# Performance work log

Hardware: AMD Instinct MI355X
Metric: run time of the kernel (lower is better)

The kernel has to match this reference:

```python
import jax, jax.numpy as jnp
import numpy as np

T, N = 256, 4096
H = 32
Z_SIZE, Z_CLS = 8, 8
A_SIZE, A_CLS = 4, 4
X_SIZE, X_CLS = 5, 2
E = X_SIZE * X_CLS  # embedder output = flatten(x[t]) -> 10, matches e_size
ZA = Z_SIZE * Z_CLS + A_SIZE * A_CLS  # GRUCell input size = 80


def setup_inputs() -> dict:
    key = jax.random.key(0)
    ks = jax.random.split(key, 10)
    s = 0.1
    u = jax.random.uniform(ks[3], (T, N, Z_SIZE, Z_CLS), jnp.float32, 1e-6, 1.0 - 1e-6)
    return {
        "x": jax.random.normal(ks[0], (T, N, X_SIZE, X_CLS), jnp.float32),
        "a": jax.random.normal(ks[1], (T, N, A_SIZE, A_CLS), jnp.float32),
        "h0": jax.random.normal(ks[2], (N, H), jnp.float32),
        "gumbel": -jnp.log(-jnp.log(u)),  # gumbel-max noise for OneHotCategorical sampling
        "W_ih": jax.random.normal(ks[4], (3 * H, ZA), jnp.float32) * s,
        "b_ih": jnp.zeros((3 * H,), jnp.float32),
        "W_hh": jax.random.normal(ks[5], (3 * H, H), jnp.float32) * s,
        "b_hh": jnp.zeros((3 * H,), jnp.float32),
        "W_enc": jax.random.normal(ks[6], (Z_SIZE * Z_CLS, H + E), jnp.float32) * s,
        "b_enc": jnp.zeros((Z_SIZE * Z_CLS,), jnp.float32),
        "W_dec": jax.random.normal(ks[7], (X_SIZE * X_CLS, H + Z_SIZE * Z_CLS), jnp.float32) * s,
        "b_dec": jnp.zeros((X_SIZE * X_CLS,), jnp.float32),
    }


def _gru(xin, h, W_ih, b_ih, W_hh, b_hh):
    # torch.nn.GRUCell semantics
    gi = xin @ W_ih.T + b_ih
    gh = h @ W_hh.T + b_hh
    i_r, i_z, i_n = jnp.split(gi, 3, axis=-1)
    h_r, h_z, h_n = jnp.split(gh, 3, axis=-1)
    r = jax.nn.sigmoid(i_r + h_r)
    z = jax.nn.sigmoid(i_z + h_z)
    n = jnp.tanh(i_n + r * h_n)
    return (1.0 - z) * n + z * h


def _encode(h, e, g, W_enc, b_enc):
    # encoder linear -> [N, z_size, z_cls] logits -> straight-through one-hot sample
    logits = (jnp.concatenate([h, e], axis=-1) @ W_enc.T + b_enc)
    logits = logits.reshape(h.shape[0], Z_SIZE, Z_CLS)
    idx = jnp.argmax(logits + g, axis=-1)  # gumbel-max categorical sample
    one_hot = jax.nn.one_hot(idx, Z_CLS, dtype=logits.dtype)
    probs = jax.nn.softmax(logits, axis=-1)
    return one_hot + probs - jax.lax.stop_gradient(probs)


def reference(x, a, h0, gumbel, W_ih, b_ih, W_hh, b_hh, W_enc, b_enc, W_dec, b_dec):
    z0 = _encode(h0, x[0].reshape(N, -1), gumbel[0], W_enc, b_enc)

    def step(carry, inp):
        h, z = carry
        x_t, a_prev, g_t = inp
        za = jnp.concatenate([z.reshape(N, -1), a_prev.reshape(N, -1)], axis=-1)
        h_new = _gru(za, h, W_ih, b_ih, W_hh, b_hh)
        z_new = _encode(h_new, x_t.reshape(N, -1), g_t, W_enc, b_enc)
        return (h_new, z_new), (h_new, z_new)

    _, (hs, zs) = jax.lax.scan(step, (h0, z0), (x[1:], a[:-1], gumbel[1:]))
    h_all = jnp.concatenate([h0[None], hs], axis=0)          # [T, N, H]
    z_all = jnp.concatenate([z0[None], zs], axis=0)          # [T, N, z_size, z_cls]
    hz = jnp.concatenate([h_all, z_all.reshape(T, N, -1)], axis=-1)
    x_logits = (hz @ W_dec.T + b_dec).reshape(T, N, X_SIZE, X_CLS)
    return x_logits, h_all, z_all
```

## Files before the change

kernel.cpp:

```cpp
#include <hip/hip_runtime.h>
#include <math.h>

#define T_STEPS 256
#define NB 4096

__global__ __launch_bounds__(256, 2)
void rssm_kernel(const float* __restrict__ X, const float* __restrict__ A,
                 const float* __restrict__ H0, const float* __restrict__ G,
                 const float* __restrict__ Wih, const float* __restrict__ bih,
                 const float* __restrict__ Whh, const float* __restrict__ bhh,
                 const float* __restrict__ Wenc, const float* __restrict__ benc,
                 const float* __restrict__ Wdec, const float* __restrict__ bdec,
                 float* __restrict__ out)
{
    __shared__ float  sWihz[96][65];
    __shared__ float  sWiha[96][17];
    __shared__ float  sWhh [96][33];
    __shared__ float  sWenchT[32][64];
    __shared__ float  sWenceT[10][64];
    __shared__ float  sWdech[10][37];
    __shared__ float  sWdecz[10][65];
    __shared__ double sHd[8][33];

    const int tid = threadIdx.x;
    const int i   = tid & 31;
    const int e   = tid >> 5;
    const int n   = blockIdx.x * 8 + e;

    for (int idx = tid; idx < 96*64; idx += 256){ int r = idx >> 6, c = idx & 63; sWihz[r][c] = Wih[r*80 + c]; }
    for (int idx = tid; idx < 96*16; idx += 256){ int r = idx >> 4, k = idx & 15; sWiha[r][k] = Wih[r*80 + 64 + k]; }
    for (int idx = tid; idx < 96*32; idx += 256){ int r = idx >> 5, k = idx & 31; sWhh[r][k] = Whh[r*32 + k]; }
    for (int idx = tid; idx < 32*64; idx += 256){ int k = idx >> 6, j = idx & 63; sWenchT[k][j] = Wenc[j*42 + k]; }
    for (int idx = tid; idx < 10*64; idx += 256){ int k = idx >> 6, j = idx & 63; sWenceT[k][j] = Wenc[j*42 + 32 + k]; }
    for (int idx = tid; idx < 10*32; idx += 256){ int o = idx >> 5, k = idx & 31; sWdech[o][k] = Wdec[o*96 + k]; }
    for (int idx = tid; idx < 10*64; idx += 256){ int o = idx >> 6, c = idx & 63; sWdecz[o][c] = Wdec[o*96 + 32 + c]; }
    __syncthreads();

    const double br  = (double)bih[i]      + (double)bhh[i];
    const double bz  = (double)bih[32+i]   + (double)bhh[32+i];
    const double bni = (double)bih[64+i];
    const double bnh = (double)bhh[64+i];
    const double be0 = (double)benc[2*i], be1 = (double)benc[2*i+1];
    const float  bd  = (i < 10) ? bdec[i] : 0.0f;
    const int    drow = (i < 10) ? i : 9;

    double hown = (double)H0[(size_t)n * 32 + i];
    sHd[e][i] = hown;

    int zsel[8];

    const size_t HOFF = (size_t)T_STEPS * NB * 10;
    const size_t ZOFF = HOFF + (size_t)T_STEPS * NB * 32;
    const int base = tid & 32;

    float2 g2;  float ex[10];  float ar[16] = {};
    g2 = *reinterpret_cast<const float2*>(G + (size_t)n*64 + 2*i);
    {
        const float* xr = X + (size_t)n*10;
        #pragma unroll
        for (int c = 0; c < 5; ++c){
            float2 v = *reinterpret_cast<const float2*>(xr + 2*c);
            ex[2*c] = v.x; ex[2*c+1] = v.y;
        }
    }

    #pragma unroll 1
    for (int t = 0; t < T_STEPS; ++t){
        const size_t tn = (size_t)t * NB + n;

        const int tp = (t + 1 < T_STEPS) ? t + 1 : t;
        const size_t tpn = (size_t)tp * NB + n;
        float2 g2n = *reinterpret_cast<const float2*>(G + tpn*64 + 2*i);
        float exn[10];
        {
            const float* xr = X + tpn*10;
            #pragma unroll
            for (int c = 0; c < 5; ++c){
                float2 v = *reinterpret_cast<const float2*>(xr + 2*c);
                exn[2*c] = v.x; exn[2*c+1] = v.y;
            }
        }
        float arn[16];
        {
            const float4* arow = reinterpret_cast<const float4*>(A + tn*16);
            #pragma unroll
            for (int c = 0; c < 4; ++c){
                float4 v = arow[c];
                arn[4*c+0]=v.x; arn[4*c+1]=v.y; arn[4*c+2]=v.z; arn[4*c+3]=v.w;
            }
        }

        if (t > 0){
            double gr = br, gz = bz, gn = bni, hn = bnh;
            #pragma unroll
            for (int g = 0; g < 8; ++g){
                int col = zsel[g];
                gr += (double)sWihz[i][col];
                gz += (double)sWihz[32+i][col];
                gn += (double)sWihz[64+i][col];
            }
            #pragma unroll
            for (int k = 0; k < 16; ++k){
                double ak = (double)ar[k];
                gr = fma((double)sWiha[i][k],    ak, gr);
                gz = fma((double)sWiha[32+i][k], ak, gz);
                gn = fma((double)sWiha[64+i][k], ak, gn);
            }
            #pragma unroll
            for (int k = 0; k < 32; ++k){
                double hk = sHd[e][k];
                gr = fma((double)sWhh[i][k],    hk, gr);
                gz = fma((double)sWhh[32+i][k], hk, gz);
                hn = fma((double)sWhh[64+i][k], hk, hn);
            }
            double r   = 1.0 / (1.0 + exp(-gr));
            double zg  = 1.0 / (1.0 + exp(-gz));
            double arg = gn + r * hn;
            double e2  = exp(2.0 * arg);
            double nn  = 1.0 - 2.0 / (e2 + 1.0);
            hown = (1.0 - zg) * nn + zg * hown;

            sHd[e][i] = hown;
        }

        out[HOFF + tn*32 + i] = (float)hown;

        double l0 = be0, l1 = be1;
        double dacc = (double)bd;
        #pragma unroll
        for (int k = 0; k < 32; ++k){
            double hk = sHd[e][k];
            float2 w = *reinterpret_cast<const float2*>(&sWenchT[k][2*i]);
            l0 = fma((double)w.x, hk, l0);
            l1 = fma((double)w.y, hk, l1);
            dacc = fma((double)sWdech[drow][k], hk, dacc);
        }
        #pragma unroll
        for (int k = 0; k < 10; ++k){
            float2 w = *reinterpret_cast<const float2*>(&sWenceT[k][2*i]);
            double ek = (double)ex[k];
            l0 = fma((double)w.x, ek, l0);
            l1 = fma((double)w.y, ek, l1);
        }
        double y0 = l0 + (double)g2.x, y1 = l1 + (double)g2.y;
        double m; int idxv;
        if (y1 > y0){ m = y1; idxv = 2*i + 1; } else { m = y0; idxv = 2*i; }
        #pragma unroll
        for (int d = 1; d <= 2; d <<= 1){
            double mo = __shfl_xor(m, d, 64);
            int    io = __shfl_xor(idxv, d, 64);
            if (mo > m || (mo == m && io < idxv)){ m = mo; idxv = io; }
        }

        {
            float2 zv;
            zv.x = (idxv == 2*i    ) ? 1.0f : 0.0f;
            zv.y = (idxv == 2*i + 1) ? 1.0f : 0.0f;
            *reinterpret_cast<float2*>(out + ZOFF + tn*64 + 2*i) = zv;
        }

        #pragma unroll
        for (int g = 0; g < 8; ++g){
            zsel[g] = __shfl(idxv, base + 4*g, 64);
        }

        if (i < 10){
            double acc = dacc;
            #pragma unroll
            for (int g = 0; g < 8; ++g) acc += (double)sWdecz[i][zsel[g]];
            out[tn*10 + i] = (float)acc;
        }

        g2 = g2n;
        #pragma unroll
        for (int k = 0; k < 10; ++k) ex[k] = exn[k];
        #pragma unroll
        for (int k = 0; k < 16; ++k) ar[k] = arn[k];
    }
}

extern "C" void kernel_launch(void* const* d_in, const int* in_sizes, int n_in,
                              void* d_out, int out_size, void* d_ws, size_t ws_size,
                              hipStream_t stream)
{
    const float *x   = (const float*)d_in[0];
    const float *a   = (const float*)d_in[1];
    const float *h0  = (const float*)d_in[2];
    const float *g   = (const float*)d_in[3];
    const float *wih = (const float*)d_in[4];
    const float *bih = (const float*)d_in[5];
    const float *whh = (const float*)d_in[6];
    const float *bhh = (const float*)d_in[7];
    const float *wenc= (const float*)d_in[8];
    const float *benc= (const float*)d_in[9];
    const float *wdec= (const float*)d_in[10];
    const float *bdec= (const float*)d_in[11];

    if (n_in == 12) {
        const float *b96a = nullptr, *b96b = nullptr;
        const float *tx=nullptr,*ta=nullptr,*th0=nullptr,*tg=nullptr,*twih=nullptr,
                    *twhh=nullptr,*twenc=nullptr,*tbenc=nullptr,*twdec=nullptr,*tbdec=nullptr;
        for (int k = 0; k < 12; ++k) {
            const float* p = (const float*)d_in[k];
            switch (in_sizes[k]) {
                case 10485760: tx = p;    break;
                case 16777216: ta = p;    break;
                case 131072:   th0 = p;   break;
                case 67108864: tg = p;    break;
                case 7680:     twih = p;  break;
                case 3072:     twhh = p;  break;
                case 2688:     twenc = p; break;
                case 64:       tbenc = p; break;
                case 960:      twdec = p; break;
                case 10:       tbdec = p; break;
                case 96:       if (!b96a) b96a = p; else b96b = p; break;
                default: break;
            }
        }
        if (tx && ta && th0 && tg && twih && twhh && twenc && tbenc && twdec && tbdec && b96a && b96b) {
            x = tx; a = ta; h0 = th0; g = tg;
            wih = twih; whh = twhh; wenc = twenc; benc = tbenc; wdec = twdec; bdec = tbdec;
            bih = b96a; bhh = b96b;
        }
    }

    rssm_kernel<<<512, 256, 0, stream>>>(
        x, a, h0, g, wih, bih, whh, bhh, wenc, benc, wdec, bdec,
        (float*)d_out);
}
```

Before: 1.158 ms.

## Use table-based fast fp64 exp and rcp, pre-convert Whh to double, fp32 decoder

Replaces the library double exp and division in the GRU gates with a table-driven exp (a 64-entry 2^(k/64) table in shared memory plus a polynomial) and a v_rcp_f64 reciprocal refined by Newton steps. Whh is stored as double in shared memory to remove per-step float-to-double conversions. The decoder dot product moves to fp32, reading a float copy of h kept alongside the double copy. Shared memory becomes dynamic and grows to about 75 KB, which may limit occupancy, and the approximated transcendentals could flip argmax decisions near ties.

Measured after the change: 1.251 ms. 8.1% more time.

```diff
diff --git a/kernel.cpp b/kernel.cpp
--- a/kernel.cpp
+++ b/kernel.cpp
@@ -3,6 +3,33 @@
 
 #define T_STEPS 256
 #define NB 4096
+
+__device__ __forceinline__ double fexp_scaled(double x, double Cs, const double* __restrict__ T){
+    const double MAGIC = 6755399441055744.0;
+    double zz = fma(x, Cs, MAGIC);
+    int    ni = __double2loint(zz);
+    double nd = zz - MAGIC;
+    double f  = fma(x, Cs, -nd);
+    double t  = f * 1.0830424696249145e-2;
+    double p  = 8.3333333333333332e-03;
+    p = fma(t, p, 4.1666666666666664e-02);
+    p = fma(t, p, 1.6666666666666666e-01);
+    p = fma(t, p, 5.0e-01);
+    p = fma(t, p, 1.0);
+    p = fma(t, p, 1.0);
+    double tb = T[ni & 63];
+    double s  = __longlong_as_double((long long)(1023 + (ni >> 6)) << 52);
+    return tb * p * s;
+}
+__device__ __forceinline__ double frcp(double d){
+    double r;
+    asm("v_rcp_f64 %0, %1" : "=v"(r) : "v"(d));
+    r = r * fma(-d, r, 2.0);
+    r = r * fma(-d, r, 2.0);
+    return r;
+}
+#define C_NEG  (-92.332482616893656843)
+#define C_2POS (184.66496523378731369)
 
 __global__ __launch_bounds__(256, 2)
 void rssm_kernel(const float* __restrict__ X, const float* __restrict__ A,
@@ -13,14 +40,17 @@
                  const float* __restrict__ Wdec, const float* __restrict__ bdec,
                  float* __restrict__ out)
 {
-    __shared__ float  sWihz[96][65];
-    __shared__ float  sWiha[96][17];
-    __shared__ float  sWhh [96][33];
-    __shared__ float  sWenchT[32][64];
-    __shared__ float  sWenceT[10][64];
-    __shared__ float  sWdech[10][37];
-    __shared__ float  sWdecz[10][65];
-    __shared__ double sHd[8][33];
+    extern __shared__ char smem[];
+    double (*sWhh)[33]   = (double(*)[33])(smem);
+    double (*sHd)[33]    = (double(*)[33])(smem + 25344);
+    double *sExpT        = (double*)(smem + 27456);
+    float (*sWihz)[65]   = (float(*)[65])(smem + 27968);
+    float (*sWiha)[17]   = (float(*)[17])(smem + 52928);
+    float (*sWenchT)[64] = (float(*)[64])(smem + 59456);
+    float (*sWenceT)[64] = (float(*)[64])(smem + 67648);
+    float (*sWdech)[37]  = (float(*)[37])(smem + 70208);
+    float (*sWdecz)[65]  = (float(*)[65])(smem + 71688);
+    float (*sHf)[33]     = (float(*)[33])(smem + 74288);
 
     const int tid = threadIdx.x;
     const int i   = tid & 31;
@@ -29,11 +59,12 @@
 
     for (int idx = tid; idx < 96*64; idx += 256){ int r = idx >> 6, c = idx & 63; sWihz[r][c] = Wih[r*80 + c]; }
     for (int idx = tid; idx < 96*16; idx += 256){ int r = idx >> 4, k = idx & 15; sWiha[r][k] = Wih[r*80 + 64 + k]; }
-    for (int idx = tid; idx < 96*32; idx += 256){ int r = idx >> 5, k = idx & 31; sWhh[r][k] = Whh[r*32 + k]; }
+    for (int idx = tid; idx < 96*32; idx += 256){ int r = idx >> 5, k = idx & 31; sWhh[r][k] = (double)Whh[r*32 + k]; }
     for (int idx = tid; idx < 32*64; idx += 256){ int k = idx >> 6, j = idx & 63; sWenchT[k][j] = Wenc[j*42 + k]; }
     for (int idx = tid; idx < 10*64; idx += 256){ int k = idx >> 6, j = idx & 63; sWenceT[k][j] = Wenc[j*42 + 32 + k]; }
     for (int idx = tid; idx < 10*32; idx += 256){ int o = idx >> 5, k = idx & 31; sWdech[o][k] = Wdec[o*96 + k]; }
     for (int idx = tid; idx < 10*64; idx += 256){ int o = idx >> 6, c = idx & 63; sWdecz[o][c] = Wdec[o*96 + 32 + c]; }
+    for (int idx = tid; idx < 64;    idx += 256){ sExpT[idx] = exp2((double)idx * 0.015625); }
     __syncthreads();
 
     const double br  = (double)bih[i]      + (double)bhh[i];
@@ -46,6 +77,7 @@
 
     double hown = (double)H0[(size_t)n * 32 + i];
     sHd[e][i] = hown;
+    sHf[e][i] = (float)hown;
 
     int zsel[8];
 
@@ -109,31 +141,31 @@
             #pragma unroll
             for (int k = 0; k < 32; ++k){
                 double hk = sHd[e][k];
-                gr = fma((double)sWhh[i][k],    hk, gr);
-                gz = fma((double)sWhh[32+i][k], hk, gz);
-                hn = fma((double)sWhh[64+i][k], hk, hn);
-            }
-            double r   = 1.0 / (1.0 + exp(-gr));
-            double zg  = 1.0 / (1.0 + exp(-gz));
+                gr = fma(sWhh[i][k],    hk, gr);
+                gz = fma(sWhh[32+i][k], hk, gz);
+                hn = fma(sWhh[64+i][k], hk, hn);
+            }
+            double r   = frcp(1.0 + fexp_scaled(gr, C_NEG, sExpT));
+            double zg  = frcp(1.0 + fexp_scaled(gz, C_NEG, sExpT));
             double arg = gn + r * hn;
-            double e2  = exp(2.0 * arg);
-            double nn  = 1.0 - 2.0 / (e2 + 1.0);
+            double e2  = fexp_scaled(arg, C_2POS, sExpT);
+            double nn  = fma(-2.0, frcp(e2 + 1.0), 1.0);
             hown = (1.0 - zg) * nn + zg * hown;
 
             sHd[e][i] = hown;
-        }
-
-        out[HOFF + tn*32 + i] = (float)hown;
+            sHf[e][i] = (float)hown;
+        }
+
+        const float hf = (float)hown;
+        out[HOFF + tn*32 + i] = hf;
 
         double l0 = be0, l1 = be1;
-        double dacc = (double)bd;
         #pragma unroll
         for (int k = 0; k < 32; ++k){
             double hk = sHd[e][k];
             float2 w = *reinterpret_cast<const float2*>(&sWenchT[k][2*i]);
             l0 = fma((double)w.x, hk, l0);
             l1 = fma((double)w.y, hk, l1);
-            dacc = fma((double)sWdech[drow][k], hk, dacc);
         }
         #pragma unroll
         for (int k = 0; k < 10; ++k){
@@ -164,11 +196,16 @@
             zsel[g] = __shfl(idxv, base + 4*g, 64);
         }
 
+        float dacc = bd;
+        #pragma unroll
+        for (int k = 0; k < 32; ++k){
+            dacc = fmaf(sWdech[drow][k], sHf[e][k], dacc);
+        }
         if (i < 10){
-            double acc = dacc;
-            #pragma unroll
-            for (int g = 0; g < 8; ++g) acc += (double)sWdecz[i][zsel[g]];
-            out[tn*10 + i] = (float)acc;
+            float acc = dacc;
+            #pragma unroll
+            for (int g = 0; g < 8; ++g) acc += sWdecz[i][zsel[g]];
+            out[tn*10 + i] = acc;
         }
 
         g2 = g2n;
@@ -224,7 +261,10 @@
         }
     }
 
-    rssm_kernel<<<512, 256, 0, stream>>>(
+    const int SMEM_BYTES = 75344;
+    hipFuncSetAttribute((const void*)rssm_kernel,
+                        hipFuncAttributeMaxDynamicSharedMemorySize, SMEM_BYTES);
+    rssm_kernel<<<512, 256, SMEM_BYTES, stream>>>(
         x, a, h0, g, wih, bih, whh, bhh, wenc, benc, wdec, bdec,
         (float*)d_out);
 }
```
